# Performance work log

Hardware: AMD Instinct MI355X
Metric: run time of the kernel (lower is better)

The kernel has to match this reference:

```python
import jax, jax.numpy as jnp
import numpy as np

B, S, H = 2, 2048, 1024
NH, HD = 16, 64  # num heads, head dim
EPS = 1e-12

def layernorm(x, g, b):
    mu = jnp.mean(x, axis=-1, keepdims=True)
    var = jnp.mean(jnp.square(x - mu), axis=-1, keepdims=True)
    return (x - mu) / jnp.sqrt(var + EPS) * g + b

def setup_inputs() -> dict:
    key = jax.random.key(0)
    ks = jax.random.split(key, 6)
    sd = 0.02
    return {
        "x": jax.random.normal(ks[0], (B, S, H), jnp.float32),
        "ln1_g": jnp.ones((H,), jnp.float32),
        "ln1_b": jnp.zeros((H,), jnp.float32),
        "w_qkv": jax.random.normal(ks[1], (H, 3 * H), jnp.float32) * sd,
        "b_qkv": jnp.zeros((3 * H,), jnp.float32),
        "w_dense": jax.random.normal(ks[2], (H, H), jnp.float32) * sd,
        "b_dense": jnp.zeros((H,), jnp.float32),
        "ln2_g": jnp.ones((H,), jnp.float32),
        "ln2_b": jnp.zeros((H,), jnp.float32),
        "w_fc1": jax.random.normal(ks[3], (H, 2 * H), jnp.float32) * sd,
        "w_fc2": jax.random.normal(ks[4], (2 * H, H), jnp.float32) * sd,
        "b_fc2": jnp.zeros((H,), jnp.float32),
    }

def reference(x, ln1_g, ln1_b, w_qkv, b_qkv, w_dense, b_dense,
              ln2_g, ln2_b, w_fc1, w_fc2, b_fc2):
    b, s, h = x.shape
    qkv = layernorm(x, ln1_g, ln1_b) @ w_qkv + b_qkv          # (b, s, 3h)
    q, k, v = jnp.split(qkv, 3, axis=-1)
    # (b, s, h) -> (b, nh, s, hd)
    reshape = lambda t: t.reshape(b, s, NH, HD).transpose(0, 2, 1, 3)
    q, k, v = reshape(q), reshape(k), reshape(v)
    scores = jnp.einsum('bhqd,bhkd->bhqk', q, k) / jnp.sqrt(jnp.float32(HD))
    causal = jnp.tril(jnp.ones((s, s), dtype=bool))
    scores = jnp.where(causal, scores, -jnp.inf)
    probs = jax.nn.softmax(scores, axis=-1)
    attn = jnp.einsum('bhqk,bhkd->bhqd', probs, v)            # (b, nh, s, hd)
    attn = attn.transpose(0, 2, 1, 3).reshape(b, s, h)
    out = x + (attn @ w_dense + b_dense)
    m = layernorm(out, ln2_g, ln2_b)
    mlp = jax.nn.gelu(m @ w_fc1, approximate=False) @ w_fc2 + b_fc2
    return out + mlp
```

## Files before the change

### kernel.cpp

```cpp
#include <hip/hip_runtime.h>
#include <hip/hip_bf16.h>

typedef __bf16 bf16x8 __attribute__((ext_vector_type(8)));
typedef float  f32x4  __attribute__((ext_vector_type(4)));

typedef __attribute__((address_space(3))) unsigned int as3_u32;
typedef __attribute__((address_space(1))) unsigned int as1_u32;

__device__ __forceinline__ void gld_lds16(const void* gptr, void* lptr){
  __builtin_amdgcn_global_load_lds((const as1_u32*)gptr, (as3_u32*)lptr, 16, 0, 0);
}

__global__ __launch_bounds__(256) void transpose_all(
    const float* __restrict__ w_qkv, const float* __restrict__ w_dense,
    const float* __restrict__ w_fc1, const float* __restrict__ w_fc2,
    __bf16* __restrict__ oqkv, __bf16* __restrict__ oden,
    __bf16* __restrict__ ofc1, __bf16* __restrict__ ofc2){
  __shared__ float tile[32][33];
  int idx = blockIdx.x;
  const float* in; __bf16* out; int R, C;
  if (idx < 3072){ in = w_qkv;  out = oqkv; R = 1024; C = 3072; }
  else if (idx < 4096){ idx -= 3072; in = w_dense; out = oden; R = 1024; C = 1024; }
  else if (idx < 6144){ idx -= 4096; in = w_fc1;  out = ofc1; R = 1024; C = 2048; }
  else { idx -= 6144; in = w_fc2;  out = ofc2; R = 2048; C = 1024; }
  const int ntx = C >> 5;
  const int c0 = (idx % ntx)*32, r0 = (idx / ntx)*32;
  const int tx = threadIdx.x, ty = threadIdx.y;
  #pragma unroll
  for (int i=0;i<32;i+=8)
    tile[ty+i][tx] = in[(size_t)(r0+ty+i)*C + c0+tx];
  __syncthreads();
  #pragma unroll
  for (int i=0;i<32;i+=8)
    out[(size_t)(c0+ty+i)*R + r0+tx] = (__bf16)tile[tx][ty+i];
}

__global__ __launch_bounds__(256) void ln_kernel(const float* __restrict__ x, const float* __restrict__ g,
                                                 const float* __restrict__ b, __bf16* __restrict__ out){
  const int row = blockIdx.x, t = threadIdx.x;
  const float4 v = ((const float4*)(x + (size_t)row*1024))[t];
  float s = v.x+v.y+v.z+v.w;
  #pragma unroll
  for (int m=1;m<64;m<<=1) s += __shfl_xor(s, m);
  __shared__ float red[8];
  if ((t&63)==0) red[t>>6] = s;
  __syncthreads();
  const float mu = (red[0]+red[1]+red[2]+red[3]) * (1.f/1024.f);
  const float d0=v.x-mu, d1=v.y-mu, d2=v.z-mu, d3=v.w-mu;
  float sq = d0*d0+d1*d1+d2*d2+d3*d3;
  #pragma unroll
  for (int m=1;m<64;m<<=1) sq += __shfl_xor(sq, m);
  if ((t&63)==0) red[4+(t>>6)] = sq;
  __syncthreads();
  const float var = (red[4]+red[5]+red[6]+red[7]) * (1.f/1024.f);
  const float inv = rsqrtf(var + 1e-12f);
  const float4 gv = ((const float4*)g)[t];
  const float4 bv = ((const float4*)b)[t];
  union { __bf16 h[4]; uint2 u; } pk;
  pk.h[0]=(__bf16)(d0*inv*gv.x+bv.x); pk.h[1]=(__bf16)(d1*inv*gv.y+bv.y);
  pk.h[2]=(__bf16)(d2*inv*gv.z+bv.z); pk.h[3]=(__bf16)(d3*inv*gv.w+bv.w);
  *(uint2*)(out + (size_t)row*1024 + t*4) = pk.u;
}

template<int MODE>
__global__ __launch_bounds__(256) void gemm_bt(
    const __bf16* __restrict__ A, const __bf16* __restrict__ Bt,
    const float* __restrict__ bias, const float* __restrict__ resid,
    float* __restrict__ outF, __bf16* __restrict__ outB,
    __bf16* __restrict__ qO, __bf16* __restrict__ kO, __bf16* __restrict__ vtO,
    int M, int N, int K)
{
  __shared__ __align__(16) __bf16 As[2][128*32];
  __shared__ __align__(16) __bf16 Bs[2][128*32];
  const int tid = threadIdx.x;
  const int lane = tid & 63, wave = tid >> 6;
  const int wr = wave >> 1, wc = wave & 1;
  const int l15 = lane & 15, lg = lane >> 4;
  const int bm = blockIdx.x, bn = blockIdx.y;
  const __bf16* Ab = A  + (size_t)bm*128*K;
  const __bf16* Bb = Bt + (size_t)bn*128*K;
  f32x4 acc[4][4] = {};
  const int r0 = tid >> 2;
  const int c0 = (tid & 3) * 8;

  auto stage = [&](int kt, int b){
    const int k0 = kt*32;
    char* dA = (char*)&As[b][0] + wave*1024;
    char* dB = (char*)&Bs[b][0] + wave*1024;
    gld_lds16(Ab + (size_t)r0*K      + k0 + c0, dA);
    gld_lds16(Ab + (size_t)(r0+64)*K + k0 + c0, dA + 4096);
    gld_lds16(Bb + (size_t)r0*K      + k0 + c0, dB);
    gld_lds16(Bb + (size_t)(r0+64)*K + k0 + c0, dB + 4096);
  };

  const int nk = K >> 5;
  stage(0, 0);
  __syncthreads();
  for (int kt = 0; kt < nk; ++kt){
    const int b = kt & 1;
    if (kt+1 < nk) stage(kt+1, b^1);
    bf16x8 af[4], bfv[4];
    #pragma unroll
    for (int i=0;i<4;++i){
      af[i]  = *(const bf16x8*)&As[b][(wr*64 + i*16 + l15)*32 + lg*8];
      bfv[i] = *(const bf16x8*)&Bs[b][(wc*64 + i*16 + l15)*32 + lg*8];
    }
    #pragma unroll
    for (int i=0;i<4;++i)
      #pragma unroll
      for (int j=0;j<4;++j)
        acc[i][j] = __builtin_amdgcn_mfma_f32_16x16x32_bf16(af[i], bfv[j], acc[i][j], 0,0,0);
    __syncthreads();
  }
  #pragma unroll
  for (int i=0;i<4;++i){
    #pragma unroll
    for (int j=0;j<4;++j){
      const int col = bn*128 + wc*64 + j*16 + l15;
      float bv;
      if constexpr (MODE==2) bv = 0.f; else bv = bias[col];
      #pragma unroll
      for (int r=0;r<4;++r){
        const int row = bm*128 + wr*64 + i*16 + lg*4 + r;
        float v = acc[i][j][r] + bv;
        if constexpr (MODE==0){
          const int b_ = row >> 11, s_ = row & 2047;
          if (col < 1024){
            const int h = col>>6, d = col&63;
            qO[((size_t)(b_*16+h)*2048 + s_)*64 + d] = (__bf16)v;
          } else if (col < 2048){
            const int h = (col-1024)>>6, d = (col-1024)&63;
            kO[((size_t)(b_*16+h)*2048 + s_)*64 + d] = (__bf16)v;
          } else {
            const int h = (col-2048)>>6, d = (col-2048)&63;
            vtO[((size_t)(b_*16+h)*64 + d)*2048 + s_] = (__bf16)v;
          }
        } else if constexpr (MODE==1){
          outF[(size_t)row*N + col] = v + resid[(size_t)row*N + col];
        } else {
          const float gl = 0.5f*v*(1.f + erff(v*0.70710678118f));
          outB[(size_t)row*N + col] = (__bf16)gl;
        }
      }
    }
  }
}

__global__ __launch_bounds__(512, 4) void attn_kernel(
    const __bf16* __restrict__ Q, const __bf16* __restrict__ K,
    const __bf16* __restrict__ Vt, __bf16* __restrict__ out)
{
  __shared__ __align__(16) __bf16 Ks[2][128*64];
  __shared__ __align__(16) __bf16 Vs[2][2][64*64];
  __shared__ __align__(16) __bf16 Pl[8][16*64];
  const int tid = threadIdx.x;
  const int lane = tid & 63, wave = tid >> 6;
  const int l15 = lane & 15, lg = lane >> 4;
  const int bh = blockIdx.y;
  const int nqb = (int)gridDim.x;
  const int qblk = (bh & 16) ? (int)blockIdx.x : (nqb - 1 - (int)blockIdx.x);
  const int qb = qblk * 128;
  const int qw = qb + wave*16;
  const __bf16* Qh = Q + (size_t)bh*2048*64;
  const char*  Khc = (const char*)(K  + (size_t)bh*2048*64);
  const char*  Vhc = (const char*)(Vt + (size_t)bh*64*2048);

  bf16x8 qf[2];
  #pragma unroll
  for (int f=0;f<2;++f){
    bf16x8 t8 = *(const bf16x8*)&Qh[(size_t)(qw + l15)*64 + f*32 + lg*8];
    #pragma unroll
    for (int j=0;j<8;++j) t8[j] = (__bf16)((float)t8[j] * 0.125f);
    qf[f] = t8;
  }

  f32x4 oacc[4] = {};
  float mrun = -1e30f, lrun = 0.f;

  const int swz_st = (((lane&7) ^ (lane>>3)) << 4);
  const int rswz = ((l15 & 7) << 4);
  char* Pw = (char*)&Pl[wave][0];

  const int krow = wave*16 + (lane>>3);
  const int kh   = wave & 1;
  const int dgrp = wave >> 1;
  const int vrow = dgrp*16 + (lane>>3);

  const int nst = qblk + 1;

  {
    gld_lds16(Khc + (size_t)krow*128 + swz_st,     (char*)&Ks[0][0] + wave*2048);
    gld_lds16(Khc + (size_t)(krow+8)*128 + swz_st, (char*)&Ks[0][0] + wave*2048 + 1024);
    const char* s = Vhc + kh*128 + swz_st;
    gld_lds16(s + (size_t)vrow*4096,     (char*)&Vs[0][kh][0] + dgrp*2048);
    gld_lds16(s + (size_t)(vrow+8)*4096, (char*)&Vs[0][kh][0] + dgrp*2048 + 1024);
  }
  __syncthreads();

  for (int st = 0; st < nst; ++st){
    const int cur = st & 1;
    const int kv0 = st*128;
    if (st+1 < nst){
      const size_t nkv0 = (size_t)(kv0 + 128);
      gld_lds16(Khc + (nkv0 + krow)*128 + swz_st,     (char*)&Ks[cur^1][0] + wave*2048);
      gld_lds16(Khc + (nkv0 + krow + 8)*128 + swz_st, (char*)&Ks[cur^1][0] + wave*2048 + 1024);
      const char* s = Vhc + nkv0*2 + kh*128 + swz_st;
      gld_lds16(s + (size_t)vrow*4096,     (char*)&Vs[cur^1][kh][0] + dgrp*2048);
      gld_lds16(s + (size_t)(vrow+8)*4096, (char*)&Vs[cur^1][kh][0] + dgrp*2048 + 1024);
    }
    if (kv0 <= qw + 15){
      const char* Kb = (const char*)&Ks[cur][0];
      f32x4 sc[8];
      #pragma unroll
      for (int t=0;t<8;++t) sc[t] = f32x4{0.f,0.f,0.f,0.f};
      #pragma unroll
      for (int t=0;t<8;++t){
        const int row = t*16 + l15;
        bf16x8 k0 = *(const bf16x8*)(Kb + row*128 + ((lg*16)      ^ rswz));
        bf16x8 k1 = *(const bf16x8*)(Kb + row*128 + ((64 + lg*16) ^ rswz));
        sc[t] = __builtin_amdgcn_mfma_f32_16x16x32_bf16(k0, qf[0], sc[t], 0,0,0);
        sc[t] = __builtin_amdgcn_mfma_f32_16x16x32_bf16(k1, qf[1], sc[t], 0,0,0);
      }
      if (kv0 + 127 > qw){
        const int q = qw + l15;
        #pragma unroll
        for (int t=0;t<8;++t)
          #pragma unroll
          for (int r=0;r<4;++r)
            if (kv0 + t*16 + lg*4 + r > q) sc[t][r] = -1e30f;
      }
      f32x4 mm;
      #pragma unroll
      for (int r=0;r<4;++r){
        float a = fmaxf(fmaxf(sc[0][r],sc[1][r]), fmaxf(sc[2][r],sc[3][r]));
        float b = fmaxf(fmaxf(sc[4][r],sc[5][r]), fmaxf(sc[6][r],sc[7][r]));
        mm[r] = fmaxf(a,b);
      }
      float mx = fmaxf(fmaxf(mm[0],mm[1]), fmaxf(mm[2],mm[3]));
      mx = fmaxf(mx, __shfl_xor(mx, 16));
      mx = fmaxf(mx, __shfl_xor(mx, 32));
      const float nm = fmaxf(mrun, mx);
      const float co = exp2f((mrun - nm) * 1.44269504f);
      #pragma unroll
      for (int t=0;t<8;++t)
        #pragma unroll
        for (int r=0;r<4;++r)
          sc[t][r] = exp2f((sc[t][r] - nm) * 1.44269504f);
      f32x4 ss;
      #pragma unroll
      for (int r=0;r<4;++r){
        float a = (sc[0][r]+sc[1][r]) + (sc[2][r]+sc[3][r]);
        float b = (sc[4][r]+sc[5][r]) + (sc[6][r]+sc[7][r]);
        ss[r] = a + b;
      }
      float rs = (ss[0]+ss[1]) + (ss[2]+ss[3]);
      rs += __shfl_xor(rs, 16);
      rs += __shfl_xor(rs, 32);
      lrun = lrun*co + rs;
      mrun = nm;
      float cor[4];
      #pragma unroll
      for (int r=0;r<4;++r) cor[r] = __shfl(co, lg*4+r);
      #pragma unroll
      for (int c=0;c<4;++c)
        #pragma unroll
        for (int r=0;r<4;++r)
          oacc[c][r] *= cor[r];
      #pragma unroll
      for (int h=0; h<2; ++h){
        #pragma unroll
        for (int t=0;t<4;++t){
          union { __bf16 hh[4]; uint2 u; } pk4;
          pk4.hh[0] = (__bf16)sc[h*4+t][0];
          pk4.hh[1] = (__bf16)sc[h*4+t][1];
          pk4.hh[2] = (__bf16)sc[h*4+t][2];
          pk4.hh[3] = (__bf16)sc[h*4+t][3];
          *(uint2*)(Pw + l15*128 + ((t*32 + lg*8) ^ rswz)) = pk4.u;
        }
        const char* Vb = (const char*)&Vs[cur][h][0];
        #pragma unroll
        for (int f=0;f<2;++f){
          bf16x8 pa = *(const bf16x8*)(Pw + l15*128 + ((f*64 + lg*16) ^ rswz));
          #pragma unroll
          for (int c=0;c<4;++c){
            bf16x8 vf = *(const bf16x8*)(Vb + (c*16+l15)*128 + ((f*64 + lg*16) ^ rswz));
            oacc[c] = __builtin_amdgcn_mfma_f32_16x16x32_bf16(pa, vf, oacc[c], 0,0,0);
          }
        }
      }
    }
    __syncthreads();
  }

  const int b_ = bh >> 4, h_ = bh & 15;
  float lr[4];
  #pragma unroll
  for (int r=0;r<4;++r) lr[r] = __shfl(lrun, lg*4+r);
  #pragma unroll
  for (int c=0;c<4;++c)
    #pragma unroll
    for (int r=0;r<4;++r){
      const int row = qw + lg*4 + r;
      out[((size_t)(b_*2048 + row))*1024 + h_*64 + c*16 + l15] = (__bf16)(oacc[c][r] / lr[r]);
    }
}

extern "C" void kernel_launch(void* const* d_in, const int* in_sizes, int n_in,
                              void* d_out, int out_size, void* d_ws, size_t ws_size,
                              hipStream_t stream) {
  const float* x      = (const float*)d_in[0];
  const float* ln1_g  = (const float*)d_in[1];
  const float* ln1_b  = (const float*)d_in[2];
  const float* w_qkv  = (const float*)d_in[3];
  const float* b_qkv  = (const float*)d_in[4];
  const float* w_dense= (const float*)d_in[5];
  const float* b_dense= (const float*)d_in[6];
  const float* ln2_g  = (const float*)d_in[7];
  const float* ln2_b  = (const float*)d_in[8];
  const float* w_fc1  = (const float*)d_in[9];
  const float* w_fc2  = (const float*)d_in[10];
  const float* b_fc2  = (const float*)d_in[11];

  char* ws = (char*)d_ws;
  __bf16* wqkvT  = (__bf16*)(ws + 0);
  __bf16* wdenT  = (__bf16*)(ws + 6291456);
  __bf16* wfc1T  = (__bf16*)(ws + 8388608);
  __bf16* wfc2T  = (__bf16*)(ws + 12582912);
  __bf16* xn     = (__bf16*)(ws + 16777216);
  __bf16* Qb     = (__bf16*)(ws + 25165824);
  __bf16* Kb     = (__bf16*)(ws + 33554432);
  __bf16* Vtb    = (__bf16*)(ws + 41943040);
  __bf16* attnb  = (__bf16*)(ws + 50331648);
  float*  outf   = (float*) (ws + 58720256);
  __bf16* mb     = (__bf16*)(ws + 75497472);
  __bf16* h1b    = (__bf16*)(ws + 83886080);

  transpose_all<<<8192, dim3(32,8), 0, stream>>>(w_qkv, w_dense, w_fc1, w_fc2,
                                                 wqkvT, wdenT, wfc1T, wfc2T);
  ln_kernel<<<4096, 256, 0, stream>>>(x, ln1_g, ln1_b, xn);
  gemm_bt<0><<<dim3(32,24), 256, 0, stream>>>(xn, wqkvT, b_qkv, nullptr,
                                              nullptr, nullptr, Qb, Kb, Vtb, 4096, 3072, 1024);
  attn_kernel<<<dim3(16,32), 512, 0, stream>>>(Qb, Kb, Vtb, attnb);
  gemm_bt<1><<<dim3(32,8), 256, 0, stream>>>(attnb, wdenT, b_dense, x,
                                             outf, nullptr, nullptr, nullptr, nullptr, 4096, 1024, 1024);
  ln_kernel<<<4096, 256, 0, stream>>>(outf, ln2_g, ln2_b, mb);
  gemm_bt<2><<<dim3(32,16), 256, 0, stream>>>(mb, wfc1T, nullptr, nullptr,
                                              nullptr, h1b, nullptr, nullptr, nullptr, 4096, 2048, 1024);
  gemm_bt<1><<<dim3(32,8), 256, 0, stream>>>(h1b, wfc2T, b_fc2, outf,
                                             (float*)d_out, nullptr, nullptr, nullptr, nullptr, 4096, 1024, 2048);
}
```

Baseline: 195.4 us.

## Read V directly from global memory, skip rescale via lazy max threshold

Drops the LDS staging buffers for the transposed V tile and has each wave load V fragments straight from global memory into registers for the PV MFMA. This frees LDS, and the occupancy hint rises from 4 to 6 blocks. The online softmax now only rescales the accumulator and running sum when the new max exceeds the old by more than a threshold, which saves exp and multiply work. The per-wave causal skip check is removed, so fully masked tiles are computed anyway, and V reads lose LDS reuse across waves.

```diff
diff --git a/kernel.cpp b/kernel.cpp
--- a/kernel.cpp
+++ b/kernel.cpp
@@ -146,12 +146,11 @@
   }
 }
 
-__global__ __launch_bounds__(512, 4) void attn_kernel(
+__global__ __launch_bounds__(512, 6) void attn_kernel(
     const __bf16* __restrict__ Q, const __bf16* __restrict__ K,
     const __bf16* __restrict__ Vt, __bf16* __restrict__ out)
 {
   __shared__ __align__(16) __bf16 Ks[2][128*64];
-  __shared__ __align__(16) __bf16 Vs[2][2][64*64];
   __shared__ __align__(16) __bf16 Pl[8][16*64];
   const int tid = threadIdx.x;
   const int lane = tid & 63, wave = tid >> 6;
@@ -180,21 +179,12 @@
   const int swz_st = (((lane&7) ^ (lane>>3)) << 4);
   const int rswz = ((l15 & 7) << 4);
   char* Pw = (char*)&Pl[wave][0];
-
   const int krow = wave*16 + (lane>>3);
-  const int kh   = wave & 1;
-  const int dgrp = wave >> 1;
-  const int vrow = dgrp*16 + (lane>>3);
 
   const int nst = qblk + 1;
 
-  {
-    gld_lds16(Khc + (size_t)krow*128 + swz_st,     (char*)&Ks[0][0] + wave*2048);
-    gld_lds16(Khc + (size_t)(krow+8)*128 + swz_st, (char*)&Ks[0][0] + wave*2048 + 1024);
-    const char* s = Vhc + kh*128 + swz_st;
-    gld_lds16(s + (size_t)vrow*4096,     (char*)&Vs[0][kh][0] + dgrp*2048);
-    gld_lds16(s + (size_t)(vrow+8)*4096, (char*)&Vs[0][kh][0] + dgrp*2048 + 1024);
-  }
+  gld_lds16(Khc + (size_t)krow*128 + swz_st,     (char*)&Ks[0][0] + wave*2048);
+  gld_lds16(Khc + (size_t)(krow+8)*128 + swz_st, (char*)&Ks[0][0] + wave*2048 + 1024);
   __syncthreads();
 
   for (int st = 0; st < nst; ++st){
@@ -204,11 +194,8 @@
       const size_t nkv0 = (size_t)(kv0 + 128);
       gld_lds16(Khc + (nkv0 + krow)*128 + swz_st,     (char*)&Ks[cur^1][0] + wave*2048);
       gld_lds16(Khc + (nkv0 + krow + 8)*128 + swz_st, (char*)&Ks[cur^1][0] + wave*2048 + 1024);
-      const char* s = Vhc + nkv0*2 + kh*128 + swz_st;
-      gld_lds16(s + (size_t)vrow*4096,     (char*)&Vs[cur^1][kh][0] + dgrp*2048);
-      gld_lds16(s + (size_t)(vrow+8)*4096, (char*)&Vs[cur^1][kh][0] + dgrp*2048 + 1024);
-    }
-    if (kv0 <= qw + 15){
+    }
+    {
       const char* Kb = (const char*)&Ks[cur][0];
       f32x4 sc[8];
       #pragma unroll
@@ -239,13 +226,26 @@
       float mx = fmaxf(fmaxf(mm[0],mm[1]), fmaxf(mm[2],mm[3]));
       mx = fmaxf(mx, __shfl_xor(mx, 16));
       mx = fmaxf(mx, __shfl_xor(mx, 32));
-      const float nm = fmaxf(mrun, mx);
-      const float co = exp2f((mrun - nm) * 1.44269504f);
+      if (!__all(mx <= mrun + 8.0f)){
+        const float nm = fmaxf(mrun, mx);
+        const float co = exp2f((mrun - nm) * 1.44269504f);
+        lrun *= co;
+        float cor[4];
+        #pragma unroll
+        for (int r=0;r<4;++r) cor[r] = __shfl(co, lg*4+r);
+        #pragma unroll
+        for (int c=0;c<4;++c)
+          #pragma unroll
+          for (int r=0;r<4;++r)
+            oacc[c][r] *= cor[r];
+        mrun = nm;
+      }
+      const float mb = mrun * 1.44269504f;
       #pragma unroll
       for (int t=0;t<8;++t)
         #pragma unroll
         for (int r=0;r<4;++r)
-          sc[t][r] = exp2f((sc[t][r] - nm) * 1.44269504f);
+          sc[t][r] = exp2f(sc[t][r]*1.44269504f - mb);
       f32x4 ss;
       #pragma unroll
       for (int r=0;r<4;++r){
@@ -256,36 +256,34 @@
       float rs = (ss[0]+ss[1]) + (ss[2]+ss[3]);
       rs += __shfl_xor(rs, 16);
       rs += __shfl_xor(rs, 32);
-      lrun = lrun*co + rs;
-      mrun = nm;
-      float cor[4];
-      #pragma unroll
-      for (int r=0;r<4;++r) cor[r] = __shfl(co, lg*4+r);
-      #pragma unroll
-      for (int c=0;c<4;++c)
-        #pragma unroll
-        for (int r=0;r<4;++r)
-          oacc[c][r] *= cor[r];
+      lrun += rs;
+      uint2 pw[8];
+      #pragma unroll
+      for (int t=0;t<8;++t){
+        union { __bf16 hh[4]; uint2 u; } pk4;
+        pk4.hh[0] = (__bf16)sc[t][0];
+        pk4.hh[1] = (__bf16)sc[t][1];
+        pk4.hh[2] = (__bf16)sc[t][2];
+        pk4.hh[3] = (__bf16)sc[t][3];
+        pw[t] = pk4.u;
+      }
       #pragma unroll
       for (int h=0; h<2; ++h){
         #pragma unroll
-        for (int t=0;t<4;++t){
-          union { __bf16 hh[4]; uint2 u; } pk4;
-          pk4.hh[0] = (__bf16)sc[h*4+t][0];
-          pk4.hh[1] = (__bf16)sc[h*4+t][1];
-          pk4.hh[2] = (__bf16)sc[h*4+t][2];
-          pk4.hh[3] = (__bf16)sc[h*4+t][3];
-          *(uint2*)(Pw + l15*128 + ((t*32 + lg*8) ^ rswz)) = pk4.u;
-        }
-        const char* Vb = (const char*)&Vs[cur][h][0];
+        for (int t=0;t<4;++t)
+          *(uint2*)(Pw + l15*128 + ((t*32 + lg*8) ^ rswz)) = pw[h*4+t];
+        const char* Vg = Vhc + (size_t)(kv0 + h*64)*2;
         #pragma unroll
         for (int f=0;f<2;++f){
+          bf16x8 vf0 = *(const bf16x8*)(Vg + (size_t)(0*16+l15)*4096 + f*64 + lg*16);
+          bf16x8 vf1 = *(const bf16x8*)(Vg + (size_t)(1*16+l15)*4096 + f*64 + lg*16);
+          bf16x8 vf2 = *(const bf16x8*)(Vg + (size_t)(2*16+l15)*4096 + f*64 + lg*16);
+          bf16x8 vf3 = *(const bf16x8*)(Vg + (size_t)(3*16+l15)*4096 + f*64 + lg*16);
           bf16x8 pa = *(const bf16x8*)(Pw + l15*128 + ((f*64 + lg*16) ^ rswz));
-          #pragma unroll
-          for (int c=0;c<4;++c){
-            bf16x8 vf = *(const bf16x8*)(Vb + (c*16+l15)*128 + ((f*64 + lg*16) ^ rswz));
-            oacc[c] = __builtin_amdgcn_mfma_f32_16x16x32_bf16(pa, vf, oacc[c], 0,0,0);
-          }
+          oacc[0] = __builtin_amdgcn_mfma_f32_16x16x32_bf16(pa, vf0, oacc[0], 0,0,0);
+          oacc[1] = __builtin_amdgcn_mfma_f32_16x16x32_bf16(pa, vf1, oacc[1], 0,0,0);
+          oacc[2] = __builtin_amdgcn_mfma_f32_16x16x32_bf16(pa, vf2, oacc[2], 0,0,0);
+          oacc[3] = __builtin_amdgcn_mfma_f32_16x16x32_bf16(pa, vf3, oacc[3], 0,0,0);
         }
       }
     }
```

Measured after the change: 266.7 us. 1.36x slower.

## Add 128x64 GEMM tile for N=1024 projections and lazy softmax rescaling

Applied to the files above, without the earlier changes.

Adds a separate gemm_bt64 kernel with 128x64 output tiles for the dense and fc2 projections (N=1024). This doubles the grid from 256 to 512 blocks so the GPU's compute units are better filled, at the cost of less B-tile reuse per block. In attention, the running-max rescale of the output accumulator is skipped unless some row's max grows by more than 8 (natural-log units), which removes per-tile exp and multiply work. The risk is larger exponent values before normalisation, bounded by about e^8 in fp32/bf16.

```diff
diff --git a/kernel.cpp b/kernel.cpp
--- a/kernel.cpp
+++ b/kernel.cpp
@@ -65,8 +65,8 @@
 template<int MODE>
 __global__ __launch_bounds__(256) void gemm_bt(
     const __bf16* __restrict__ A, const __bf16* __restrict__ Bt,
-    const float* __restrict__ bias, const float* __restrict__ resid,
-    float* __restrict__ outF, __bf16* __restrict__ outB,
+    const float* __restrict__ bias,
+    __bf16* __restrict__ outB,
     __bf16* __restrict__ qO, __bf16* __restrict__ kO, __bf16* __restrict__ vtO,
     int M, int N, int K)
 {
@@ -135,12 +135,71 @@
             const int h = (col-2048)>>6, d = (col-2048)&63;
             vtO[((size_t)(b_*16+h)*64 + d)*2048 + s_] = (__bf16)v;
           }
-        } else if constexpr (MODE==1){
-          outF[(size_t)row*N + col] = v + resid[(size_t)row*N + col];
         } else {
           const float gl = 0.5f*v*(1.f + erff(v*0.70710678118f));
           outB[(size_t)row*N + col] = (__bf16)gl;
         }
+      }
+    }
+  }
+}
+
+__global__ __launch_bounds__(256) void gemm_bt64(
+    const __bf16* __restrict__ A, const __bf16* __restrict__ Bt,
+    const float* __restrict__ bias, const float* __restrict__ resid,
+    float* __restrict__ outF, int M, int N, int K)
+{
+  __shared__ __align__(16) __bf16 As[2][128*32];
+  __shared__ __align__(16) __bf16 Bs[2][64*32];
+  const int tid = threadIdx.x;
+  const int lane = tid & 63, wave = tid >> 6;
+  const int l15 = lane & 15, lg = lane >> 4;
+  const int bm = blockIdx.x, bn = blockIdx.y;
+  const __bf16* Ab = A  + (size_t)bm*128*K;
+  const __bf16* Bb = Bt + (size_t)bn*64*K;
+  f32x4 acc[2][4] = {};
+  const int r0 = tid >> 2;
+  const int c0 = (tid & 3) * 8;
+
+  auto stage = [&](int kt, int b){
+    const int k0 = kt*32;
+    char* dA = (char*)&As[b][0] + wave*1024;
+    char* dB = (char*)&Bs[b][0] + wave*1024;
+    gld_lds16(Ab + (size_t)r0*K      + k0 + c0, dA);
+    gld_lds16(Ab + (size_t)(r0+64)*K + k0 + c0, dA + 4096);
+    gld_lds16(Bb + (size_t)r0*K      + k0 + c0, dB);
+  };
+
+  const int nk = K >> 5;
+  stage(0, 0);
+  __syncthreads();
+  for (int kt = 0; kt < nk; ++kt){
+    const int b = kt & 1;
+    if (kt+1 < nk) stage(kt+1, b^1);
+    bf16x8 af[2], bfv[4];
+    #pragma unroll
+    for (int i=0;i<2;++i)
+      af[i]  = *(const bf16x8*)&As[b][(wave*32 + i*16 + l15)*32 + lg*8];
+    #pragma unroll
+    for (int j=0;j<4;++j)
+      bfv[j] = *(const bf16x8*)&Bs[b][(j*16 + l15)*32 + lg*8];
+    #pragma unroll
+    for (int i=0;i<2;++i)
+      #pragma unroll
+      for (int j=0;j<4;++j)
+        acc[i][j] = __builtin_amdgcn_mfma_f32_16x16x32_bf16(af[i], bfv[j], acc[i][j], 0,0,0);
+    __syncthreads();
+  }
+  #pragma unroll
+  for (int i=0;i<2;++i){
+    #pragma unroll
+    for (int j=0;j<4;++j){
+      const int col = bn*64 + j*16 + l15;
+      const float bv = bias[col];
+      #pragma unroll
+      for (int r=0;r<4;++r){
+        const int row = bm*128 + wave*32 + i*16 + lg*4 + r;
+        outF[(size_t)row*N + col] = acc[i][j][r] + bv + resid[(size_t)row*N + col];
       }
     }
   }
@@ -239,13 +298,26 @@
       float mx = fmaxf(fmaxf(mm[0],mm[1]), fmaxf(mm[2],mm[3]));
       mx = fmaxf(mx, __shfl_xor(mx, 16));
       mx = fmaxf(mx, __shfl_xor(mx, 32));
-      const float nm = fmaxf(mrun, mx);
-      const float co = exp2f((mrun - nm) * 1.44269504f);
+      if (!__all(mx <= mrun + 8.0f)){
+        const float nm = fmaxf(mrun, mx);
+        const float co = exp2f((mrun - nm) * 1.44269504f);
+        lrun *= co;
+        float cor[4];
+        #pragma unroll
+        for (int r=0;r<4;++r) cor[r] = __shfl(co, lg*4+r);
+        #pragma unroll
+        for (int c=0;c<4;++c)
+          #pragma unroll
+          for (int r=0;r<4;++r)
+            oacc[c][r] *= cor[r];
+        mrun = nm;
+      }
+      const float mb = mrun * 1.44269504f;
       #pragma unroll
       for (int t=0;t<8;++t)
         #pragma unroll
         for (int r=0;r<4;++r)
-          sc[t][r] = exp2f((sc[t][r] - nm) * 1.44269504f);
+          sc[t][r] = exp2f(sc[t][r]*1.44269504f - mb);
       f32x4 ss;
       #pragma unroll
       for (int r=0;r<4;++r){
@@ -256,16 +328,7 @@
       float rs = (ss[0]+ss[1]) + (ss[2]+ss[3]);
       rs += __shfl_xor(rs, 16);
       rs += __shfl_xor(rs, 32);
-      lrun = lrun*co + rs;
-      mrun = nm;
-      float cor[4];
-      #pragma unroll
-      for (int r=0;r<4;++r) cor[r] = __shfl(co, lg*4+r);
-      #pragma unroll
-      for (int c=0;c<4;++c)
-        #pragma unroll
-        for (int r=0;r<4;++r)
-          oacc[c][r] *= cor[r];
+      lrun += rs;
       #pragma unroll
       for (int h=0; h<2; ++h){
         #pragma unroll
@@ -338,14 +401,14 @@
   transpose_all<<<8192, dim3(32,8), 0, stream>>>(w_qkv, w_dense, w_fc1, w_fc2,
                                                  wqkvT, wdenT, wfc1T, wfc2T);
   ln_kernel<<<4096, 256, 0, stream>>>(x, ln1_g, ln1_b, xn);
-  gemm_bt<0><<<dim3(32,24), 256, 0, stream>>>(xn, wqkvT, b_qkv, nullptr,
-                                              nullptr, nullptr, Qb, Kb, Vtb, 4096, 3072, 1024);
+  gemm_bt<0><<<dim3(32,24), 256, 0, stream>>>(xn, wqkvT, b_qkv,
+                                              nullptr, Qb, Kb, Vtb, 4096, 3072, 1024);
   attn_kernel<<<dim3(16,32), 512, 0, stream>>>(Qb, Kb, Vtb, attnb);
-  gemm_bt<1><<<dim3(32,8), 256, 0, stream>>>(attnb, wdenT, b_dense, x,
-                                             outf, nullptr, nullptr, nullptr, nullptr, 4096, 1024, 1024);
+  gemm_bt64<<<dim3(32,16), 256, 0, stream>>>(attnb, wdenT, b_dense, x,
+                                             outf, 4096, 1024, 1024);
   ln_kernel<<<4096, 256, 0, stream>>>(outf, ln2_g, ln2_b, mb);
-  gemm_bt<2><<<dim3(32,16), 256, 0, stream>>>(mb, wfc1T, nullptr, nullptr,
-                                              nullptr, h1b, nullptr, nullptr, nullptr, 4096, 2048, 1024);
-  gemm_bt<1><<<dim3(32,8), 256, 0, stream>>>(h1b, wfc2T, b_fc2, outf,
-                                             (float*)d_out, nullptr, nullptr, nullptr, nullptr, 4096, 1024, 2048);
-}
+  gemm_bt<2><<<dim3(32,16), 256, 0, stream>>>(mb, wfc1T, nullptr,
+                                              h1b, nullptr, nullptr, nullptr, 4096, 2048, 1024);
+  gemm_bt64<<<dim3(32,16), 256, 0, stream>>>(h1b, wfc2T, b_fc2, outf,
+                                             (float*)d_out, 4096, 1024, 2048);
+}
```

New measurement: 192.4 us. No clear change (-1.5%).
